# Kernel optimization log

Measured on AMD Instinct MI355X. Metric: run time of the kernel, lower is better.

## Reference

```python
import jax, jax.numpy as jnp
import numpy as np

B, S, E, H, D = 2, 2048, 512, 8, 64
NEG = -1e10


def setup_inputs() -> dict:
    key = jax.random.key(0)
    k1, k2, k3, k4, k5, k6 = jax.random.split(key, 6)
    inputs = jax.random.normal(k1, (B, S, E), dtype=jnp.float32)
    keys = jax.random.normal(k2, (B, S, H, D), dtype=jnp.float32)
    values = jax.random.normal(k3, (B, S, H, D), dtype=jnp.float32)
    # xavier-uniform style scale for square weights
    lim = float(np.sqrt(6.0 / (E + H * D)))
    query_weights = jax.random.uniform(k4, (E, H * D), minval=-lim, maxval=lim, dtype=jnp.float32)
    output_weights = jax.random.uniform(k5, (H * D, E), minval=-lim, maxval=lim, dtype=jnp.float32)
    mask = jax.random.randint(k6, (B, S, S), 0, 2).astype(jnp.bool_)
    return {"inputs": inputs, "keys": keys, "values": values,
            "query_weights": query_weights, "output_weights": output_weights,
            "mask": mask}


def reference(inputs, keys, values, query_weights, output_weights, mask):
    # project queries: (B,S,E) @ (E,H*D) -> (B,S,H,D)
    q = jnp.matmul(inputs, query_weights).reshape(B, S, H, D)
    # scores: (B,H,Sq,Sk)
    scores = jnp.einsum('bqhd,bkhd->bhqk', q, keys) / jnp.sqrt(jnp.float32(D))
    # masked_fill(mask, -1e10); mask broadcasts over heads
    scores = jnp.where(mask[:, None, :, :], jnp.float32(NEG), scores)
    probs = jax.nn.softmax(scores, axis=-1)
    # (B,H,Sq,Sk) x (B,Sk,H,D) -> (B,Sq,H,D)
    out = jnp.einsum('bhqk,bkhd->bqhd', probs, values)
    out = out.reshape(B, S, H * D)
    return jnp.matmul(out, output_weights)
```

## Files before the change

kernel.cpp:

```cpp
#include <hip/hip_runtime.h>
#include <hip/hip_bf16.h>

namespace {

constexpr int B = 2, S = 2048, E = 512, H = 8, D = 64, HD = 512;
constexpr float SL = 0.125f * 1.44269504f;
constexpr int PLD = 40;

typedef __attribute__((ext_vector_type(8))) short bf16x8;
typedef __attribute__((ext_vector_type(4))) unsigned short u16x4;
typedef __attribute__((ext_vector_type(4))) float f32x4;
typedef __attribute__((ext_vector_type(4))) float float4v;

__device__ __forceinline__ ushort f2b(float x) {
  __hip_bfloat16 h = __float2bfloat16(x);
  return *reinterpret_cast<const ushort*>(&h);
}

__global__ __launch_bounds__(256) void prep_fused_kernel(
    const float* __restrict__ K, const float* __restrict__ V,
    const float* __restrict__ Wq, const float* __restrict__ Wo,
    const int* __restrict__ maskp,
    ushort* __restrict__ Kbf, ushort* __restrict__ Vtbf,
    ushort* __restrict__ Wtq, ushort* __restrict__ Wto,
    uint4* __restrict__ keep4) {
  const int bid = blockIdx.x;
  const int t = threadIdx.x;
  if (bid < 512) {
    __shared__ __align__(16) ushort Vn[64][76];
    const int kt = bid & 31;
    const int bh = bid >> 5;
    const int b = bh >> 3, h = bh & 7;
    const int k0 = kt * 64;
#pragma unroll
    for (int i = 0; i < 4; ++i) {
      int c = i * 256 + t;
      int kk = c >> 4, d4 = (c & 15) * 4;
      size_t g = ((size_t)(b * 2048 + k0 + kk) * 8 + h) * 64 + d4;
      float4v kv = *(const float4v*)(K + g);
      float4v vv = *(const float4v*)(V + g);
      u16x4 kp = {f2b(kv.x), f2b(kv.y), f2b(kv.z), f2b(kv.w)};
      u16x4 vp = {f2b(vv.x), f2b(vv.y), f2b(vv.z), f2b(vv.w)};
      *(u16x4*)(Kbf + ((size_t)(bh * 2048 + k0 + kk)) * 64 + d4) = kp;
      *(u16x4*)&Vn[kk][d4] = vp;
    }
    __syncthreads();
#pragma unroll
    for (int i = 0; i < 2; ++i) {
      int c = i * 256 + t;
      int kc8 = (c & 7) * 8, d = c >> 3;
      union { ushort u[8]; bf16x8 v; } p;
#pragma unroll
      for (int j = 0; j < 8; ++j) p.u[j] = Vn[kc8 + j][d];
      *(bf16x8*)(Vtbf + ((size_t)(bh * 64 + d)) * 2048 + k0 + kc8) = p.v;
    }
  } else if (bid < 640) {
    __shared__ __align__(16) ushort T[64][68];
    const int idx = bid - 512;
    const float* Wsrc = (idx >> 6) ? Wo : Wq;
    ushort* Wdst = (idx >> 6) ? Wto : Wtq;
    const int x = idx & 63;
    const int k0 = (x & 7) * 64, n0 = (x >> 3) * 64;
#pragma unroll
    for (int i = 0; i < 4; ++i) {
      int c = i * 256 + t;
      int kk = c >> 4, n4 = (c & 15) * 4;
      float4v v = *(const float4v*)(Wsrc + (size_t)(k0 + kk) * 512 + n0 + n4);
      u16x4 p = {f2b(v.x), f2b(v.y), f2b(v.z), f2b(v.w)};
      *(u16x4*)&T[kk][n4] = p;
    }
    __syncthreads();
#pragma unroll
    for (int i = 0; i < 2; ++i) {
      int c = i * 256 + t;
      int n = c >> 3, k8 = (c & 7) * 8;
      union { ushort u[8]; bf16x8 v; } p;
#pragma unroll
      for (int j = 0; j < 8; ++j) p.u[j] = T[k8 + j][n];
      *(bf16x8*)(Wdst + (size_t)(n0 + n) * 512 + k0 + k8) = p.v;
    }
  } else {
    const int wid = (bid - 640) * 4 + (t >> 6);
    const int row = wid >> 3, c = wid & 7;
    const int lane = t & 63;
    const int4 v = *((const int4*)(maskp + (size_t)row * 2048 + c * 256) + lane);
    unsigned long long bx = __ballot(v.x == 0);
    unsigned long long by = __ballot(v.y == 0);
    unsigned long long bz = __ballot(v.z == 0);
    unsigned long long bw = __ballot(v.w == 0);
    if (lane == 0)
      keep4[(size_t)row * 16 + c * 2] = uint4{(uint)bx, (uint)by, (uint)bz, (uint)bw};
    if (lane == 32)
      keep4[(size_t)row * 16 + c * 2 + 1] =
          uint4{(uint)(bx >> 32), (uint)(by >> 32), (uint)(bz >> 32), (uint)(bw >> 32)};
  }
}

__global__ __launch_bounds__(256) void proj_out_kernel(
    const ushort* __restrict__ A, const ushort* __restrict__ Wt, float* __restrict__ C) {
  __shared__ __align__(16) ushort As[64][PLD];
  __shared__ __align__(16) ushort Ws[64][PLD];

  const int tid = threadIdx.x;
  const int lane = tid & 63;
  const int w = tid >> 6;
  const int col = lane & 15;
  const int quad = lane >> 4;
  const int m0 = blockIdx.y * 64;
  const int n0 = blockIdx.x * 64;
  const int wm = (w & 1) * 32;
  const int wn = (w >> 1) * 32;
  const int ar = tid >> 2;
  const int ak = (tid & 3) * 8;
  const int wn2 = tid >> 2;
  const int wkc = (tid & 3) * 8;

  f32x4 acc[2][2];
#pragma unroll
  for (int i = 0; i < 2; ++i)
#pragma unroll
    for (int j = 0; j < 2; ++j) acc[i][j] = f32x4{0.f, 0.f, 0.f, 0.f};

  const ushort* Ap = A + (size_t)(m0 + ar) * 512 + ak;
  const ushort* Wp = Wt + (size_t)(n0 + wn2) * 512 + wkc;
  bf16x8 apre = *(const bf16x8*)Ap;
  bf16x8 wp = *(const bf16x8*)Wp;

  for (int kt = 0; kt < 16; ++kt) {
    if (kt) __syncthreads();
    *(bf16x8*)&As[ar][ak] = apre;
    *(bf16x8*)&Ws[wn2][wkc] = wp;
    if (kt < 15) {
      const int k1 = (kt + 1) * 32;
      apre = *(const bf16x8*)(Ap + k1);
      wp = *(const bf16x8*)(Wp + k1);
    }
    __syncthreads();

    bf16x8 ah[2], wb[2];
#pragma unroll
    for (int i = 0; i < 2; ++i)
      ah[i] = *(const bf16x8*)&As[wm + i * 16 + col][quad * 8];
#pragma unroll
    for (int j = 0; j < 2; ++j)
      wb[j] = *(const bf16x8*)&Ws[wn + j * 16 + col][quad * 8];
#pragma unroll
    for (int i = 0; i < 2; ++i)
#pragma unroll
      for (int j = 0; j < 2; ++j)
        acc[i][j] = __builtin_amdgcn_mfma_f32_16x16x32_bf16(ah[i], wb[j], acc[i][j], 0, 0, 0);
  }

#pragma unroll
  for (int i = 0; i < 2; ++i)
#pragma unroll
    for (int j = 0; j < 2; ++j)
#pragma unroll
      for (int r = 0; r < 4; ++r)
        C[(size_t)(m0 + wm + i * 16 + (quad << 2) + r) * 512 + n0 + wn + j * 16 + col] =
            acc[i][j][r];
}

__global__ __launch_bounds__(256, 2) void flash_attn_kernel(
    const float* __restrict__ inp, const ushort* __restrict__ Wtq,
    const ushort* __restrict__ Kbf, const ushort* __restrict__ Vtbf,
    const uint4* __restrict__ keep4, ushort* __restrict__ Op) {
  __shared__ __align__(16) union SM {
    struct { ushort Ks[128][72]; ushort Vt[64][136]; ushort PQ[64][72]; } m;
    struct { float red[3][64][68]; float lred[3][64]; } r;
  } sm;

  const int bid = blockIdx.x;
  const int qt = bid & 31;
  const int bh = bid >> 5;
  const int b = bh >> 3, h = bh & 7;
  const int q0 = qt * 64;
  const int tid = threadIdx.x, lane = tid & 63, w = tid >> 6;
  const int col = lane & 15, quad = lane >> 4, quad4 = quad * 4;
  const int wm = (w & 1) * 32;
  const int wn = (w >> 1) * 32;

  {
    const int ar = tid >> 2;
    const int ak = (tid & 3) * 8;

    f32x4 qacc[2][2];
#pragma unroll
    for (int i = 0; i < 2; ++i)
#pragma unroll
      for (int j = 0; j < 2; ++j) qacc[i][j] = f32x4{0.f, 0.f, 0.f, 0.f};

    const float* Ap = inp + (size_t)(b * 2048 + q0 + ar) * 512 + ak;
    const ushort* Wp = Wtq + (size_t)(h * 64 + ar) * 512 + ak;
    float4v a0p = *(const float4v*)Ap;
    float4v a1p = *(const float4v*)(Ap + 4);
    bf16x8 wp = *(const bf16x8*)Wp;

    for (int kt = 0; kt < 16; ++kt) {
      if (kt) __syncthreads();
      {
        union { ushort u[8]; bf16x8 v; } ap;
        ap.u[0] = f2b(a0p.x); ap.u[1] = f2b(a0p.y); ap.u[2] = f2b(a0p.z); ap.u[3] = f2b(a0p.w);
        ap.u[4] = f2b(a1p.x); ap.u[5] = f2b(a1p.y); ap.u[6] = f2b(a1p.z); ap.u[7] = f2b(a1p.w);
        *(bf16x8*)&sm.m.PQ[ar][ak] = ap.v;
        *(bf16x8*)&sm.m.PQ[ar][40 + ak] = wp;
      }
      if (kt < 15) {
        const int k1 = (kt + 1) * 32;
        a0p = *(const float4v*)(Ap + k1);
        a1p = *(const float4v*)(Ap + k1 + 4);
        wp = *(const bf16x8*)(Wp + k1);
      }
      __syncthreads();

      bf16x8 ah[2], wb[2];
#pragma unroll
      for (int i = 0; i < 2; ++i)
        ah[i] = *(const bf16x8*)&sm.m.PQ[wm + i * 16 + col][quad * 8];
#pragma unroll
      for (int j = 0; j < 2; ++j)
        wb[j] = *(const bf16x8*)&sm.m.PQ[wn + j * 16 + col][40 + quad * 8];
#pragma unroll
      for (int i = 0; i < 2; ++i)
#pragma unroll
        for (int j = 0; j < 2; ++j)
          qacc[i][j] = __builtin_amdgcn_mfma_f32_16x16x32_bf16(ah[i], wb[j], qacc[i][j], 0, 0, 0);
    }

    __syncthreads();
#pragma unroll
    for (int i = 0; i < 2; ++i)
#pragma unroll
      for (int j = 0; j < 2; ++j)
#pragma unroll
        for (int r = 0; r < 4; ++r)
          sm.m.PQ[wm + i * 16 + quad4 + r][wn + j * 16 + col] = f2b(qacc[i][j][r]);
    __syncthreads();
  }

  bf16x8 qb[4][2];
#pragma unroll
  for (int j = 0; j < 4; ++j)
#pragma unroll
    for (int hf = 0; hf < 2; ++hf)
      qb[j][hf] = *(const bf16x8*)&sm.m.PQ[j * 16 + col][hf * 32 + quad * 8];

  f32x4 oacc[4][4];
#pragma unroll
  for (int j = 0; j < 4; ++j)
#pragma unroll
    for (int c = 0; c < 4; ++c) oacc[j][c] = f32x4{0.f, 0.f, 0.f, 0.f};
  f32x4 lacc[4];
#pragma unroll
  for (int j = 0; j < 4; ++j) lacc[j] = f32x4{0.f, 0.f, 0.f, 0.f};

  union { ushort u[8]; bf16x8 v; } onesu;
#pragma unroll
  for (int j = 0; j < 8; ++j) onesu.u[j] = 0x3F80;
  const bf16x8 onesB = onesu.v;

  const uint4* kr0 = keep4 + (size_t)(b * 2048 + q0 + col) * 16;
  const ushort* Kbase = Kbf + (size_t)bh * 2048 * 64;
  const ushort* Vbase = Vtbf + (size_t)bh * 64 * 2048;
  const int mshift = 8 * w + quad;

  bf16x8 kpre[4], vpre[4];
#pragma unroll
  for (int i = 0; i < 4; ++i) {
    int c = i * 256 + tid;
    kpre[i] = *(const bf16x8*)(Kbase + (size_t)c * 8);
    int d = c >> 4, k8 = (c & 15) * 8;
    vpre[i] = *(const bf16x8*)(Vbase + (size_t)d * 2048 + k8);
  }

  for (int kt = 0; kt < 16; ++kt) {
    if (kt) __syncthreads();
#pragma unroll
    for (int i = 0; i < 4; ++i) {
      int c = i * 256 + tid;
      *(bf16x8*)&sm.m.Ks[c >> 3][(c & 7) * 8] = kpre[i];
      int d = c >> 4, k8 = (c & 15) * 8;
      *(bf16x8*)&sm.m.Vt[d][k8] = vpre[i];
    }
    uint4 kwj[4];
#pragma unroll
    for (int j = 0; j < 4; ++j) kwj[j] = kr0[j * 256 + kt];
    if (kt < 15) {
      const int k1 = (kt + 1) * 128;
#pragma unroll
      for (int i = 0; i < 4; ++i) {
        int c = i * 256 + tid;
        kpre[i] = *(const bf16x8*)(Kbase + (size_t)k1 * 64 + c * 8);
        int d = c >> 4, k8 = (c & 15) * 8;
        vpre[i] = *(const bf16x8*)(Vbase + (size_t)d * 2048 + k1 + k8);
      }
    }
    __syncthreads();

    bf16x8 ka[2][2];
#pragma unroll
    for (int t = 0; t < 2; ++t)
#pragma unroll
      for (int hf = 0; hf < 2; ++hf)
        ka[t][hf] = *(const bf16x8*)&sm.m.Ks[w * 32 + t * 16 + col][hf * 32 + quad * 8];

    f32x4 sc[2][4];
#pragma unroll
    for (int t = 0; t < 2; ++t)
#pragma unroll
      for (int j = 0; j < 4; ++j) sc[t][j] = f32x4{0.f, 0.f, 0.f, 0.f};
#pragma unroll
    for (int t = 0; t < 2; ++t)
#pragma unroll
      for (int hf = 0; hf < 2; ++hf)
#pragma unroll
        for (int j = 0; j < 4; ++j)
          sc[t][j] = __builtin_amdgcn_mfma_f32_16x16x32_bf16(ka[t][hf], qb[j][hf], sc[t][j], 0, 0, 0);

    bf16x8 vb[4];
#pragma unroll
    for (int c = 0; c < 4; ++c)
      vb[c] = *(const bf16x8*)&sm.m.Vt[c * 16 + col][w * 32 + quad * 8];

#pragma unroll
    for (int j = 0; j < 4; ++j) {
      const uint mx_ = kwj[j].x >> mshift, my_ = kwj[j].y >> mshift,
                 mz_ = kwj[j].z >> mshift, mw_ = kwj[j].w >> mshift;
      uint Xa0, Xa1, Xb0, Xb1;
      {
        float p0 = (mx_ & 1u) ? exp2f(sc[0][j][0] * SL) : 0.f;
        float p1 = (my_ & 1u) ? exp2f(sc[0][j][1] * SL) : 0.f;
        float p2 = (mz_ & 1u) ? exp2f(sc[0][j][2] * SL) : 0.f;
        float p3 = (mw_ & 1u) ? exp2f(sc[0][j][3] * SL) : 0.f;
        __hip_bfloat162 lo = __float22bfloat162_rn(float2{p0, p1});
        __hip_bfloat162 hi = __float22bfloat162_rn(float2{p2, p3});
        Xa0 = *reinterpret_cast<uint*>(&lo);
        Xa1 = *reinterpret_cast<uint*>(&hi);
      }
      {
        float p0 = ((mx_ >> 4) & 1u) ? exp2f(sc[1][j][0] * SL) : 0.f;
        float p1 = ((my_ >> 4) & 1u) ? exp2f(sc[1][j][1] * SL) : 0.f;
        float p2 = ((mz_ >> 4) & 1u) ? exp2f(sc[1][j][2] * SL) : 0.f;
        float p3 = ((mw_ >> 4) & 1u) ? exp2f(sc[1][j][3] * SL) : 0.f;
        __hip_bfloat162 lo = __float22bfloat162_rn(float2{p0, p1});
        __hip_bfloat162 hi = __float22bfloat162_rn(float2{p2, p3});
        Xb0 = *reinterpret_cast<uint*>(&lo);
        Xb1 = *reinterpret_cast<uint*>(&hi);
      }
      auto a32 = __builtin_amdgcn_permlane32_swap(Xa0, Xb0, false, false);
      auto a16 = __builtin_amdgcn_permlane16_swap(a32[0], a32[1], false, false);
      auto b32 = __builtin_amdgcn_permlane32_swap(Xa1, Xb1, false, false);
      auto b16 = __builtin_amdgcn_permlane16_swap(b32[0], b32[1], false, false);
      union { uint u[4]; bf16x8 v; } pu;
      pu.u[0] = a16[0]; pu.u[1] = b16[0]; pu.u[2] = a16[1]; pu.u[3] = b16[1];
      const bf16x8 pa = pu.v;
      lacc[j] = __builtin_amdgcn_mfma_f32_16x16x32_bf16(pa, onesB, lacc[j], 0, 0, 0);
#pragma unroll
      for (int c = 0; c < 4; ++c)
        oacc[j][c] = __builtin_amdgcn_mfma_f32_16x16x32_bf16(pa, vb[c], oacc[j][c], 0, 0, 0);
    }
  }

  __syncthreads();
  if (w > 0) {
    const int wi = w - 1;
#pragma unroll
    for (int j = 0; j < 4; ++j)
#pragma unroll
      for (int c = 0; c < 4; ++c)
        *(f32x4*)&sm.r.red[wi][c * 16 + col][j * 16 + quad4] = oacc[j][c];
    if (col == 0)
#pragma unroll
      for (int j = 0; j < 4; ++j)
        *(f32x4*)&sm.r.lred[wi][j * 16 + quad4] = lacc[j];
  }
  __syncthreads();
  if (w == 0) {
#pragma unroll
    for (int j = 0; j < 4; ++j) {
#pragma unroll
      for (int c = 0; c < 4; ++c) {
        f32x4 s = oacc[j][c];
#pragma unroll
        for (int i = 0; i < 3; ++i)
          s += *(const f32x4*)&sm.r.red[i][c * 16 + col][j * 16 + quad4];
        oacc[j][c] = s;
      }
      f32x4 ls = lacc[j];
#pragma unroll
      for (int i = 0; i < 3; ++i)
        ls += *(const f32x4*)&sm.r.lred[i][j * 16 + quad4];
      lacc[j] = ls;
    }
#pragma unroll
    for (int j = 0; j < 4; ++j) {
#pragma unroll
      for (int c = 0; c < 4; ++c)
        *(f32x4*)&sm.r.red[0][c * 16 + col][j * 16 + quad4] = oacc[j][c];
      if (col == 0) *(f32x4*)&sm.r.lred[0][j * 16 + quad4] = lacc[j];
    }
  }
  __syncthreads();

  {
    const int q = tid >> 2, d0 = (tid & 3) * 16;
    const float inv = 1.f / sm.r.lred[0][q];
    union { ushort u[16]; bf16x8 v[2]; } ob;
#pragma unroll
    for (int dd = 0; dd < 16; ++dd)
      ob.u[dd] = f2b(sm.r.red[0][d0 + dd][q] * inv);
    ushort* dst = Op + (size_t)(b * S + q0 + q) * HD + h * D + d0;
    *(bf16x8*)dst = ob.v[0];
    *(bf16x8*)(dst + 8) = ob.v[1];
  }
}

}

extern "C" void kernel_launch(void* const* d_in, const int* in_sizes, int n_in,
                              void* d_out, int out_size, void* d_ws, size_t ws_size,
                              hipStream_t stream) {
  const float* inputs = (const float*)d_in[0];
  const float* keys   = (const float*)d_in[1];
  const float* values = (const float*)d_in[2];
  const float* wq     = (const float*)d_in[3];
  const float* wo     = (const float*)d_in[4];
  const int*   maskp  = (const int*)d_in[5];
  float* out = (float*)d_out;

  ushort* Kbf  = (ushort*)d_out;
  ushort* Vtbf = Kbf + (size_t)2097152;

  char* ws = (char*)d_ws;
  ushort* attnb = (ushort*)ws;
  uint4*  keep4 = (uint4*)(ws + (4 << 20));
  ushort* Wtq   = (ushort*)(ws + (5 << 20));
  ushort* Wto   = (ushort*)(ws + (5 << 20) + (512 << 10));

  prep_fused_kernel<<<dim3(8832), dim3(256), 0, stream>>>(keys, values, wq, wo, maskp,
                                                          Kbf, Vtbf, Wtq, Wto, keep4);
  flash_attn_kernel<<<dim3(512), dim3(256), 0, stream>>>(inputs, Wtq, Kbf, Vtbf, keep4, attnb);
  proj_out_kernel<<<dim3(8, 64), dim3(256), 0, stream>>>(attnb, Wto, out);
}
```

Measured before the change: 161.0 us.

## Halve attention query tile to 32 rows and double grid with block swizzle

The fused Q-projection and flash-attention kernel now processes 32 query rows per block instead of 64. The grid doubles to 1024 blocks and the launch-bounds occupancy target rises from 2 to 3, to fill the GPU better. Block indices are swizzled, the softmax scale is folded into Q when it is written to shared memory, the next tile's mask words are prefetched, and s_setprio is placed around the MFMA groups. The trade-off is that K/V tiles are loaded twice as often per query row, and half the threads sit idle while A is staged during the projection.

```diff
diff --git a/kernel.cpp b/kernel.cpp
--- a/kernel.cpp
+++ b/kernel.cpp
@@ -161,98 +161,92 @@
             acc[i][j][r];
 }
 
-__global__ __launch_bounds__(256, 2) void flash_attn_kernel(
+__global__ __launch_bounds__(256, 3) void flash_attn_kernel(
     const float* __restrict__ inp, const ushort* __restrict__ Wtq,
     const ushort* __restrict__ Kbf, const ushort* __restrict__ Vtbf,
     const uint4* __restrict__ keep4, ushort* __restrict__ Op) {
   __shared__ __align__(16) union SM {
-    struct { ushort Ks[128][72]; ushort Vt[64][136]; ushort PQ[64][72]; } m;
-    struct { float red[3][64][68]; float lred[3][64]; } r;
+    struct { ushort Ks[128][72]; ushort Vt[64][136]; } m;
+    ushort PQ[64][72];
+    struct { float red[3][64][40]; float lred[3][40]; } r;
   } sm;
 
-  const int bid = blockIdx.x;
-  const int qt = bid & 31;
-  const int bh = bid >> 5;
+  const int bid0 = blockIdx.x;
+  const int bid = (bid0 & 7) * 128 + (bid0 >> 3);
+  const int qt = bid & 63;
+  const int bh = bid >> 6;
   const int b = bh >> 3, h = bh & 7;
-  const int q0 = qt * 64;
+  const int q0 = qt * 32;
   const int tid = threadIdx.x, lane = tid & 63, w = tid >> 6;
   const int col = lane & 15, quad = lane >> 4, quad4 = quad * 4;
-  const int wm = (w & 1) * 32;
-  const int wn = (w >> 1) * 32;
 
   {
+    const int wmq = (w & 1) * 16;
+    const int wnq = (w >> 1) * 32;
     const int ar = tid >> 2;
     const int ak = (tid & 3) * 8;
-
-    f32x4 qacc[2][2];
-#pragma unroll
-    for (int i = 0; i < 2; ++i)
-#pragma unroll
-      for (int j = 0; j < 2; ++j) qacc[i][j] = f32x4{0.f, 0.f, 0.f, 0.f};
-
-    const float* Ap = inp + (size_t)(b * 2048 + q0 + ar) * 512 + ak;
+    const bool astage = tid < 128;
+
+    f32x4 qacc[2];
+    qacc[0] = f32x4{0.f, 0.f, 0.f, 0.f};
+    qacc[1] = f32x4{0.f, 0.f, 0.f, 0.f};
+
+    const float* Ap = inp + (size_t)(b * 2048 + q0 + (ar & 31)) * 512 + ak;
     const ushort* Wp = Wtq + (size_t)(h * 64 + ar) * 512 + ak;
-    float4v a0p = *(const float4v*)Ap;
-    float4v a1p = *(const float4v*)(Ap + 4);
+    float4v a0p{}, a1p{};
+    if (astage) { a0p = *(const float4v*)Ap; a1p = *(const float4v*)(Ap + 4); }
     bf16x8 wp = *(const bf16x8*)Wp;
 
     for (int kt = 0; kt < 16; ++kt) {
       if (kt) __syncthreads();
-      {
+      if (astage) {
         union { ushort u[8]; bf16x8 v; } ap;
         ap.u[0] = f2b(a0p.x); ap.u[1] = f2b(a0p.y); ap.u[2] = f2b(a0p.z); ap.u[3] = f2b(a0p.w);
         ap.u[4] = f2b(a1p.x); ap.u[5] = f2b(a1p.y); ap.u[6] = f2b(a1p.z); ap.u[7] = f2b(a1p.w);
-        *(bf16x8*)&sm.m.PQ[ar][ak] = ap.v;
-        *(bf16x8*)&sm.m.PQ[ar][40 + ak] = wp;
-      }
+        *(bf16x8*)&sm.PQ[ar][ak] = ap.v;
+      }
+      *(bf16x8*)&sm.PQ[ar][40 + ak] = wp;
+      __syncthreads();
       if (kt < 15) {
         const int k1 = (kt + 1) * 32;
-        a0p = *(const float4v*)(Ap + k1);
-        a1p = *(const float4v*)(Ap + k1 + 4);
+        if (astage) {
+          a0p = *(const float4v*)(Ap + k1);
+          a1p = *(const float4v*)(Ap + k1 + 4);
+        }
         wp = *(const bf16x8*)(Wp + k1);
       }
-      __syncthreads();
-
-      bf16x8 ah[2], wb[2];
-#pragma unroll
-      for (int i = 0; i < 2; ++i)
-        ah[i] = *(const bf16x8*)&sm.m.PQ[wm + i * 16 + col][quad * 8];
-#pragma unroll
-      for (int j = 0; j < 2; ++j)
-        wb[j] = *(const bf16x8*)&sm.m.PQ[wn + j * 16 + col][40 + quad * 8];
-#pragma unroll
-      for (int i = 0; i < 2; ++i)
-#pragma unroll
-        for (int j = 0; j < 2; ++j)
-          qacc[i][j] = __builtin_amdgcn_mfma_f32_16x16x32_bf16(ah[i], wb[j], qacc[i][j], 0, 0, 0);
-    }
-
-    __syncthreads();
-#pragma unroll
-    for (int i = 0; i < 2; ++i)
-#pragma unroll
-      for (int j = 0; j < 2; ++j)
-#pragma unroll
-        for (int r = 0; r < 4; ++r)
-          sm.m.PQ[wm + i * 16 + quad4 + r][wn + j * 16 + col] = f2b(qacc[i][j][r]);
-    __syncthreads();
-  }
-
-  bf16x8 qb[4][2];
-#pragma unroll
-  for (int j = 0; j < 4; ++j)
+      bf16x8 ah = *(const bf16x8*)&sm.PQ[wmq + col][quad * 8];
+      bf16x8 wb0 = *(const bf16x8*)&sm.PQ[wnq + col][40 + quad * 8];
+      bf16x8 wb1 = *(const bf16x8*)&sm.PQ[wnq + 16 + col][40 + quad * 8];
+      qacc[0] = __builtin_amdgcn_mfma_f32_16x16x32_bf16(ah, wb0, qacc[0], 0, 0, 0);
+      qacc[1] = __builtin_amdgcn_mfma_f32_16x16x32_bf16(ah, wb1, qacc[1], 0, 0, 0);
+    }
+
+    __syncthreads();
+#pragma unroll
+    for (int j = 0; j < 2; ++j)
+#pragma unroll
+      for (int r = 0; r < 4; ++r)
+        sm.PQ[wmq + quad4 + r][wnq + j * 16 + col] = f2b(qacc[j][r] * SL);
+    __syncthreads();
+  }
+
+  bf16x8 qb[2][2];
+#pragma unroll
+  for (int j = 0; j < 2; ++j)
 #pragma unroll
     for (int hf = 0; hf < 2; ++hf)
-      qb[j][hf] = *(const bf16x8*)&sm.m.PQ[j * 16 + col][hf * 32 + quad * 8];
-
-  f32x4 oacc[4][4];
-#pragma unroll
-  for (int j = 0; j < 4; ++j)
+      qb[j][hf] = *(const bf16x8*)&sm.PQ[j * 16 + col][hf * 32 + quad * 8];
+  __syncthreads();
+
+  f32x4 oacc[2][4];
+#pragma unroll
+  for (int j = 0; j < 2; ++j)
 #pragma unroll
     for (int c = 0; c < 4; ++c) oacc[j][c] = f32x4{0.f, 0.f, 0.f, 0.f};
-  f32x4 lacc[4];
-#pragma unroll
-  for (int j = 0; j < 4; ++j) lacc[j] = f32x4{0.f, 0.f, 0.f, 0.f};
+  f32x4 lacc[2];
+  lacc[0] = f32x4{0.f, 0.f, 0.f, 0.f};
+  lacc[1] = f32x4{0.f, 0.f, 0.f, 0.f};
 
   union { ushort u[8]; bf16x8 v; } onesu;
 #pragma unroll
@@ -265,6 +259,7 @@
   const int mshift = 8 * w + quad;
 
   bf16x8 kpre[4], vpre[4];
+  uint4 kwj[2];
 #pragma unroll
   for (int i = 0; i < 4; ++i) {
     int c = i * 256 + tid;
@@ -272,6 +267,8 @@
     int d = c >> 4, k8 = (c & 15) * 8;
     vpre[i] = *(const bf16x8*)(Vbase + (size_t)d * 2048 + k8);
   }
+  kwj[0] = kr0[0];
+  kwj[1] = kr0[256];
 
   for (int kt = 0; kt < 16; ++kt) {
     if (kt) __syncthreads();
@@ -282,9 +279,9 @@
       int d = c >> 4, k8 = (c & 15) * 8;
       *(bf16x8*)&sm.m.Vt[d][k8] = vpre[i];
     }
-    uint4 kwj[4];
-#pragma unroll
-    for (int j = 0; j < 4; ++j) kwj[j] = kr0[j * 256 + kt];
+    __syncthreads();
+
+    uint4 kwn0 = kwj[0], kwn1 = kwj[1];
     if (kt < 15) {
       const int k1 = (kt + 1) * 128;
 #pragma unroll
@@ -294,8 +291,9 @@
         int d = c >> 4, k8 = (c & 15) * 8;
         vpre[i] = *(const bf16x8*)(Vbase + (size_t)d * 2048 + k1 + k8);
       }
-    }
-    __syncthreads();
+      kwn0 = kr0[kt + 1];
+      kwn1 = kr0[256 + kt + 1];
+    }
 
     bf16x8 ka[2][2];
 #pragma unroll
@@ -304,18 +302,20 @@
       for (int hf = 0; hf < 2; ++hf)
         ka[t][hf] = *(const bf16x8*)&sm.m.Ks[w * 32 + t * 16 + col][hf * 32 + quad * 8];
 
-    f32x4 sc[2][4];
+    f32x4 sc[2][2];
 #pragma unroll
     for (int t = 0; t < 2; ++t)
 #pragma unroll
-      for (int j = 0; j < 4; ++j) sc[t][j] = f32x4{0.f, 0.f, 0.f, 0.f};
+      for (int j = 0; j < 2; ++j) sc[t][j] = f32x4{0.f, 0.f, 0.f, 0.f};
+    __builtin_amdgcn_s_setprio(1);
 #pragma unroll
     for (int t = 0; t < 2; ++t)
 #pragma unroll
       for (int hf = 0; hf < 2; ++hf)
 #pragma unroll
-        for (int j = 0; j < 4; ++j)
+        for (int j = 0; j < 2; ++j)
           sc[t][j] = __builtin_amdgcn_mfma_f32_16x16x32_bf16(ka[t][hf], qb[j][hf], sc[t][j], 0, 0, 0);
+    __builtin_amdgcn_s_setprio(0);
 
     bf16x8 vb[4];
 #pragma unroll
@@ -323,25 +323,26 @@
       vb[c] = *(const bf16x8*)&sm.m.Vt[c * 16 + col][w * 32 + quad * 8];
 
 #pragma unroll
-    for (int j = 0; j < 4; ++j) {
-      const uint mx_ = kwj[j].x >> mshift, my_ = kwj[j].y >> mshift,
-                 mz_ = kwj[j].z >> mshift, mw_ = kwj[j].w >> mshift;
+    for (int j = 0; j < 2; ++j) {
+      const uint4 kwv = j ? kwn1 * 0 + kwj[1] : kwj[0];
+      const uint mx_ = kwv.x >> mshift, my_ = kwv.y >> mshift,
+                 mz_ = kwv.z >> mshift, mw_ = kwv.w >> mshift;
       uint Xa0, Xa1, Xb0, Xb1;
       {
-        float p0 = (mx_ & 1u) ? exp2f(sc[0][j][0] * SL) : 0.f;
-        float p1 = (my_ & 1u) ? exp2f(sc[0][j][1] * SL) : 0.f;
-        float p2 = (mz_ & 1u) ? exp2f(sc[0][j][2] * SL) : 0.f;
-        float p3 = (mw_ & 1u) ? exp2f(sc[0][j][3] * SL) : 0.f;
+        float p0 = (mx_ & 1u) ? exp2f(sc[0][j][0]) : 0.f;
+        float p1 = (my_ & 1u) ? exp2f(sc[0][j][1]) : 0.f;
+        float p2 = (mz_ & 1u) ? exp2f(sc[0][j][2]) : 0.f;
+        float p3 = (mw_ & 1u) ? exp2f(sc[0][j][3]) : 0.f;
         __hip_bfloat162 lo = __float22bfloat162_rn(float2{p0, p1});
         __hip_bfloat162 hi = __float22bfloat162_rn(float2{p2, p3});
         Xa0 = *reinterpret_cast<uint*>(&lo);
         Xa1 = *reinterpret_cast<uint*>(&hi);
       }
       {
-        float p0 = ((mx_ >> 4) & 1u) ? exp2f(sc[1][j][0] * SL) : 0.f;
-        float p1 = ((my_ >> 4) & 1u) ? exp2f(sc[1][j][1] * SL) : 0.f;
-        float p2 = ((mz_ >> 4) & 1u) ? exp2f(sc[1][j][2] * SL) : 0.f;
-        float p3 = ((mw_ >> 4) & 1u) ? exp2f(sc[1][j][3] * SL) : 0.f;
+        float p0 = ((mx_ >> 4) & 1u) ? exp2f(sc[1][j][0]) : 0.f;
+        float p1 = ((my_ >> 4) & 1u) ? exp2f(sc[1][j][1]) : 0.f;
+        float p2 = ((mz_ >> 4) & 1u) ? exp2f(sc[1][j][2]) : 0.f;
+        float p3 = ((mw_ >> 4) & 1u) ? exp2f(sc[1][j][3]) : 0.f;
         __hip_bfloat162 lo = __float22bfloat162_rn(float2{p0, p1});
         __hip_bfloat162 hi = __float22bfloat162_rn(float2{p2, p3});
         Xb0 = *reinterpret_cast<uint*>(&lo);
@@ -354,30 +355,32 @@
       union { uint u[4]; bf16x8 v; } pu;
       pu.u[0] = a16[0]; pu.u[1] = b16[0]; pu.u[2] = a16[1]; pu.u[3] = b16[1];
       const bf16x8 pa = pu.v;
+      __builtin_amdgcn_s_setprio(1);
       lacc[j] = __builtin_amdgcn_mfma_f32_16x16x32_bf16(pa, onesB, lacc[j], 0, 0, 0);
 #pragma unroll
       for (int c = 0; c < 4; ++c)
         oacc[j][c] = __builtin_amdgcn_mfma_f32_16x16x32_bf16(pa, vb[c], oacc[j][c], 0, 0, 0);
-    }
+      __builtin_amdgcn_s_setprio(0);
+    }
+    kwj[0] = kwn0;
+    kwj[1] = kwn1;
   }
 
   __syncthreads();
   if (w > 0) {
     const int wi = w - 1;
 #pragma unroll
-    for (int j = 0; j < 4; ++j)
+    for (int j = 0; j < 2; ++j) {
 #pragma unroll
       for (int c = 0; c < 4; ++c)
         *(f32x4*)&sm.r.red[wi][c * 16 + col][j * 16 + quad4] = oacc[j][c];
-    if (col == 0)
-#pragma unroll
-      for (int j = 0; j < 4; ++j)
-        *(f32x4*)&sm.r.lred[wi][j * 16 + quad4] = lacc[j];
+      if (col == 0) *(f32x4*)&sm.r.lred[wi][j * 16 + quad4] = lacc[j];
+    }
   }
   __syncthreads();
   if (w == 0) {
 #pragma unroll
-    for (int j = 0; j < 4; ++j) {
+    for (int j = 0; j < 2; ++j) {
 #pragma unroll
       for (int c = 0; c < 4; ++c) {
         f32x4 s = oacc[j][c];
@@ -393,7 +396,7 @@
       lacc[j] = ls;
     }
 #pragma unroll
-    for (int j = 0; j < 4; ++j) {
+    for (int j = 0; j < 2; ++j) {
 #pragma unroll
       for (int c = 0; c < 4; ++c)
         *(f32x4*)&sm.r.red[0][c * 16 + col][j * 16 + quad4] = oacc[j][c];
@@ -403,15 +406,14 @@
   __syncthreads();
 
   {
-    const int q = tid >> 2, d0 = (tid & 3) * 16;
+    const int q = tid >> 3, d0 = (tid & 7) * 8;
     const float inv = 1.f / sm.r.lred[0][q];
-    union { ushort u[16]; bf16x8 v[2]; } ob;
-#pragma unroll
-    for (int dd = 0; dd < 16; ++dd)
+    union { ushort u[8]; bf16x8 v; } ob;
+#pragma unroll
+    for (int dd = 0; dd < 8; ++dd)
       ob.u[dd] = f2b(sm.r.red[0][d0 + dd][q] * inv);
     ushort* dst = Op + (size_t)(b * S + q0 + q) * HD + h * D + d0;
-    *(bf16x8*)dst = ob.v[0];
-    *(bf16x8*)(dst + 8) = ob.v[1];
+    *(bf16x8*)dst = ob.v;
   }
 }
 
@@ -439,6 +441,6 @@
 
   prep_fused_kernel<<<dim3(8832), dim3(256), 0, stream>>>(keys, values, wq, wo, maskp,
                                                           Kbf, Vtbf, Wtq, Wto, keep4);
-  flash_attn_kernel<<<dim3(512), dim3(256), 0, stream>>>(inputs, Wtq, Kbf, Vtbf, keep4, attnb);
+  flash_attn_kernel<<<dim3(1024), dim3(256), 0, stream>>>(inputs, Wtq, Kbf, Vtbf, keep4, attnb);
   proj_out_kernel<<<dim3(8, 64), dim3(256), 0, stream>>>(attnb, Wto, out);
 }
```

Result: slower. 169.7 us (+5.4%).

## Load K/V fragments directly from global into registers, drop LDS staging

Applied to the files above, without the earlier changes.

The attention loop no longer stages K and V tiles through shared memory with block-wide barriers. Each wave instead reads its MFMA fragments straight from global memory, with register double-buffering of K and mask words across iterations. The softmax scale is folded into Q when it is written to LDS, which removes a multiply per score. Block indices are also remapped so that consecutive blocks spread across batch/head. This removes LDS traffic and barriers at the cost of redundant global/L2 reads of V across waves and higher register pressure.

```diff
diff --git a/kernel.cpp b/kernel.cpp
--- a/kernel.cpp
+++ b/kernel.cpp
@@ -166,11 +166,12 @@
     const ushort* __restrict__ Kbf, const ushort* __restrict__ Vtbf,
     const uint4* __restrict__ keep4, ushort* __restrict__ Op) {
   __shared__ __align__(16) union SM {
-    struct { ushort Ks[128][72]; ushort Vt[64][136]; ushort PQ[64][72]; } m;
+    ushort PQ[64][72];
     struct { float red[3][64][68]; float lred[3][64]; } r;
   } sm;
 
-  const int bid = blockIdx.x;
+  const int bid0 = blockIdx.x;
+  const int bid = (bid0 & 7) * 64 + (bid0 >> 3);
   const int qt = bid & 31;
   const int bh = bid >> 5;
   const int b = bh >> 3, h = bh & 7;
@@ -202,8 +203,8 @@
         union { ushort u[8]; bf16x8 v; } ap;
         ap.u[0] = f2b(a0p.x); ap.u[1] = f2b(a0p.y); ap.u[2] = f2b(a0p.z); ap.u[3] = f2b(a0p.w);
         ap.u[4] = f2b(a1p.x); ap.u[5] = f2b(a1p.y); ap.u[6] = f2b(a1p.z); ap.u[7] = f2b(a1p.w);
-        *(bf16x8*)&sm.m.PQ[ar][ak] = ap.v;
-        *(bf16x8*)&sm.m.PQ[ar][40 + ak] = wp;
+        *(bf16x8*)&sm.PQ[ar][ak] = ap.v;
+        *(bf16x8*)&sm.PQ[ar][40 + ak] = wp;
       }
       if (kt < 15) {
         const int k1 = (kt + 1) * 32;
@@ -216,10 +217,10 @@
       bf16x8 ah[2], wb[2];
 #pragma unroll
       for (int i = 0; i < 2; ++i)
-        ah[i] = *(const bf16x8*)&sm.m.PQ[wm + i * 16 + col][quad * 8];
+        ah[i] = *(const bf16x8*)&sm.PQ[wm + i * 16 + col][quad * 8];
 #pragma unroll
       for (int j = 0; j < 2; ++j)
-        wb[j] = *(const bf16x8*)&sm.m.PQ[wn + j * 16 + col][40 + quad * 8];
+        wb[j] = *(const bf16x8*)&sm.PQ[wn + j * 16 + col][40 + quad * 8];
 #pragma unroll
       for (int i = 0; i < 2; ++i)
 #pragma unroll
@@ -234,7 +235,7 @@
       for (int j = 0; j < 2; ++j)
 #pragma unroll
         for (int r = 0; r < 4; ++r)
-          sm.m.PQ[wm + i * 16 + quad4 + r][wn + j * 16 + col] = f2b(qacc[i][j][r]);
+          sm.PQ[wm + i * 16 + quad4 + r][wn + j * 16 + col] = f2b(qacc[i][j][r] * SL);
     __syncthreads();
   }
 
@@ -243,7 +244,7 @@
   for (int j = 0; j < 4; ++j)
 #pragma unroll
     for (int hf = 0; hf < 2; ++hf)
-      qb[j][hf] = *(const bf16x8*)&sm.m.PQ[j * 16 + col][hf * 32 + quad * 8];
+      qb[j][hf] = *(const bf16x8*)&sm.PQ[j * 16 + col][hf * 32 + quad * 8];
 
   f32x4 oacc[4][4];
 #pragma unroll
@@ -260,88 +261,54 @@
   const bf16x8 onesB = onesu.v;
 
   const uint4* kr0 = keep4 + (size_t)(b * 2048 + q0 + col) * 16;
-  const ushort* Kbase = Kbf + (size_t)bh * 2048 * 64;
-  const ushort* Vbase = Vtbf + (size_t)bh * 64 * 2048;
+  const ushort* Kp = Kbf + (size_t)bh * 131072 + (size_t)(w * 32 + col) * 64 + quad * 8;
+  const ushort* Vp = Vtbf + (size_t)bh * 131072 + (size_t)col * 2048 + w * 32 + quad * 8;
   const int mshift = 8 * w + quad;
 
-  bf16x8 kpre[4], vpre[4];
-#pragma unroll
-  for (int i = 0; i < 4; ++i) {
-    int c = i * 256 + tid;
-    kpre[i] = *(const bf16x8*)(Kbase + (size_t)c * 8);
-    int d = c >> 4, k8 = (c & 15) * 8;
-    vpre[i] = *(const bf16x8*)(Vbase + (size_t)d * 2048 + k8);
-  }
-
-  for (int kt = 0; kt < 16; ++kt) {
-    if (kt) __syncthreads();
-#pragma unroll
-    for (int i = 0; i < 4; ++i) {
-      int c = i * 256 + tid;
-      *(bf16x8*)&sm.m.Ks[c >> 3][(c & 7) * 8] = kpre[i];
-      int d = c >> 4, k8 = (c & 15) * 8;
-      *(bf16x8*)&sm.m.Vt[d][k8] = vpre[i];
-    }
-    uint4 kwj[4];
-#pragma unroll
-    for (int j = 0; j < 4; ++j) kwj[j] = kr0[j * 256 + kt];
-    if (kt < 15) {
-      const int k1 = (kt + 1) * 128;
-#pragma unroll
-      for (int i = 0; i < 4; ++i) {
-        int c = i * 256 + tid;
-        kpre[i] = *(const bf16x8*)(Kbase + (size_t)k1 * 64 + c * 8);
-        int d = c >> 4, k8 = (c & 15) * 8;
-        vpre[i] = *(const bf16x8*)(Vbase + (size_t)d * 2048 + k1 + k8);
-      }
-    }
-    __syncthreads();
-
-    bf16x8 ka[2][2];
+  auto LOADK = [&](bf16x8 (&d)[2][2], const int kt) {
 #pragma unroll
     for (int t = 0; t < 2; ++t)
 #pragma unroll
       for (int hf = 0; hf < 2; ++hf)
-        ka[t][hf] = *(const bf16x8*)&sm.m.Ks[w * 32 + t * 16 + col][hf * 32 + quad * 8];
-
-    f32x4 sc[2][4];
-#pragma unroll
-    for (int t = 0; t < 2; ++t)
-#pragma unroll
-      for (int j = 0; j < 4; ++j) sc[t][j] = f32x4{0.f, 0.f, 0.f, 0.f};
-#pragma unroll
-    for (int t = 0; t < 2; ++t)
-#pragma unroll
-      for (int hf = 0; hf < 2; ++hf)
-#pragma unroll
-        for (int j = 0; j < 4; ++j)
-          sc[t][j] = __builtin_amdgcn_mfma_f32_16x16x32_bf16(ka[t][hf], qb[j][hf], sc[t][j], 0, 0, 0);
-
-    bf16x8 vb[4];
-#pragma unroll
-    for (int c = 0; c < 4; ++c)
-      vb[c] = *(const bf16x8*)&sm.m.Vt[c * 16 + col][w * 32 + quad * 8];
-
+        d[t][hf] = *(const bf16x8*)(Kp + kt * 8192 + t * 1024 + hf * 32);
+  };
+  auto LOADM = [&](uint4 (&d)[4], const int kt) {
+#pragma unroll
+    for (int j = 0; j < 4; ++j) d[j] = kr0[j * 256 + kt];
+  };
+  auto COMPUTE = [&](const bf16x8 (&ka)[2][2], const uint4 (&kwj)[4], const int kt) {
+    bf16x8 vv[4];
 #pragma unroll
     for (int j = 0; j < 4; ++j) {
+      f32x4 sc0 = f32x4{0.f, 0.f, 0.f, 0.f};
+      f32x4 sc1 = f32x4{0.f, 0.f, 0.f, 0.f};
+      sc0 = __builtin_amdgcn_mfma_f32_16x16x32_bf16(ka[0][0], qb[j][0], sc0, 0, 0, 0);
+      sc0 = __builtin_amdgcn_mfma_f32_16x16x32_bf16(ka[0][1], qb[j][1], sc0, 0, 0, 0);
+      sc1 = __builtin_amdgcn_mfma_f32_16x16x32_bf16(ka[1][0], qb[j][0], sc1, 0, 0, 0);
+      sc1 = __builtin_amdgcn_mfma_f32_16x16x32_bf16(ka[1][1], qb[j][1], sc1, 0, 0, 0);
+      if (j == 0) {
+#pragma unroll
+        for (int c = 0; c < 4; ++c)
+          vv[c] = *(const bf16x8*)(Vp + kt * 128 + c * 32768);
+      }
       const uint mx_ = kwj[j].x >> mshift, my_ = kwj[j].y >> mshift,
                  mz_ = kwj[j].z >> mshift, mw_ = kwj[j].w >> mshift;
       uint Xa0, Xa1, Xb0, Xb1;
       {
-        float p0 = (mx_ & 1u) ? exp2f(sc[0][j][0] * SL) : 0.f;
-        float p1 = (my_ & 1u) ? exp2f(sc[0][j][1] * SL) : 0.f;
-        float p2 = (mz_ & 1u) ? exp2f(sc[0][j][2] * SL) : 0.f;
-        float p3 = (mw_ & 1u) ? exp2f(sc[0][j][3] * SL) : 0.f;
+        float p0 = (mx_ & 1u) ? exp2f(sc0[0]) : 0.f;
+        float p1 = (my_ & 1u) ? exp2f(sc0[1]) : 0.f;
+        float p2 = (mz_ & 1u) ? exp2f(sc0[2]) : 0.f;
+        float p3 = (mw_ & 1u) ? exp2f(sc0[3]) : 0.f;
         __hip_bfloat162 lo = __float22bfloat162_rn(float2{p0, p1});
         __hip_bfloat162 hi = __float22bfloat162_rn(float2{p2, p3});
         Xa0 = *reinterpret_cast<uint*>(&lo);
         Xa1 = *reinterpret_cast<uint*>(&hi);
       }
       {
-        float p0 = ((mx_ >> 4) & 1u) ? exp2f(sc[1][j][0] * SL) : 0.f;
-        float p1 = ((my_ >> 4) & 1u) ? exp2f(sc[1][j][1] * SL) : 0.f;
-        float p2 = ((mz_ >> 4) & 1u) ? exp2f(sc[1][j][2] * SL) : 0.f;
-        float p3 = ((mw_ >> 4) & 1u) ? exp2f(sc[1][j][3] * SL) : 0.f;
+        float p0 = ((mx_ >> 4) & 1u) ? exp2f(sc1[0]) : 0.f;
+        float p1 = ((my_ >> 4) & 1u) ? exp2f(sc1[1]) : 0.f;
+        float p2 = ((mz_ >> 4) & 1u) ? exp2f(sc1[2]) : 0.f;
+        float p3 = ((mw_ >> 4) & 1u) ? exp2f(sc1[3]) : 0.f;
         __hip_bfloat162 lo = __float22bfloat162_rn(float2{p0, p1});
         __hip_bfloat162 hi = __float22bfloat162_rn(float2{p2, p3});
         Xb0 = *reinterpret_cast<uint*>(&lo);
@@ -357,8 +324,21 @@
       lacc[j] = __builtin_amdgcn_mfma_f32_16x16x32_bf16(pa, onesB, lacc[j], 0, 0, 0);
 #pragma unroll
       for (int c = 0; c < 4; ++c)
-        oacc[j][c] = __builtin_amdgcn_mfma_f32_16x16x32_bf16(pa, vb[c], oacc[j][c], 0, 0, 0);
-    }
+        oacc[j][c] = __builtin_amdgcn_mfma_f32_16x16x32_bf16(pa, vv[c], oacc[j][c], 0, 0, 0);
+    }
+  };
+
+  bf16x8 kA[2][2], kB[2][2];
+  uint4 kwA[4], kwB[4];
+  LOADK(kA, 0);
+#pragma unroll 1
+  for (int kt = 0; kt < 16; kt += 2) {
+    LOADM(kwA, kt);
+    LOADK(kB, kt + 1);
+    COMPUTE(kA, kwA, kt);
+    LOADM(kwB, kt + 1);
+    if (kt < 14) LOADK(kA, kt + 2);
+    COMPUTE(kB, kwB, kt + 1);
   }
 
   __syncthreads();
```

Result: slower. 168.4 us (+4.6%).

## Move Q projection into prep kernel and prescale Q by softmax scale

Applied to the files above, without the earlier changes.

The Q projection (inputs @ Wq) moves out of the flash attention kernel into new blocks of the prep kernel. Those blocks write Q in bf16, already multiplied by the softmax scale, in a per-head layout that the attention kernel reads straight from global memory. This removes duplicated projection work and the PQ shared buffer from attention, and drops one multiply per exp. It also adds s_setprio around the MFMA sections. The cost is an extra global round-trip for Q and a prep kernel whose Wq is transposed through shared memory with scattered ushort stores.

```diff
diff --git a/kernel.cpp b/kernel.cpp
--- a/kernel.cpp
+++ b/kernel.cpp
@@ -18,11 +18,12 @@
 }
 
 __global__ __launch_bounds__(256) void prep_fused_kernel(
+    const float* __restrict__ inp,
     const float* __restrict__ K, const float* __restrict__ V,
     const float* __restrict__ Wq, const float* __restrict__ Wo,
     const int* __restrict__ maskp,
     ushort* __restrict__ Kbf, ushort* __restrict__ Vtbf,
-    ushort* __restrict__ Wtq, ushort* __restrict__ Wto,
+    ushort* __restrict__ Wto, ushort* __restrict__ Qbf,
     uint4* __restrict__ keep4) {
   const int bid = blockIdx.x;
   const int t = threadIdx.x;
@@ -54,18 +55,15 @@
       for (int j = 0; j < 8; ++j) p.u[j] = Vn[kc8 + j][d];
       *(bf16x8*)(Vtbf + ((size_t)(bh * 64 + d)) * 2048 + k0 + kc8) = p.v;
     }
-  } else if (bid < 640) {
+  } else if (bid < 576) {
     __shared__ __align__(16) ushort T[64][68];
-    const int idx = bid - 512;
-    const float* Wsrc = (idx >> 6) ? Wo : Wq;
-    ushort* Wdst = (idx >> 6) ? Wto : Wtq;
-    const int x = idx & 63;
+    const int x = bid - 512;
     const int k0 = (x & 7) * 64, n0 = (x >> 3) * 64;
 #pragma unroll
     for (int i = 0; i < 4; ++i) {
       int c = i * 256 + t;
       int kk = c >> 4, n4 = (c & 15) * 4;
-      float4v v = *(const float4v*)(Wsrc + (size_t)(k0 + kk) * 512 + n0 + n4);
+      float4v v = *(const float4v*)(Wo + (size_t)(k0 + kk) * 512 + n0 + n4);
       u16x4 p = {f2b(v.x), f2b(v.y), f2b(v.z), f2b(v.w)};
       *(u16x4*)&T[kk][n4] = p;
     }
@@ -77,10 +75,10 @@
       union { ushort u[8]; bf16x8 v; } p;
 #pragma unroll
       for (int j = 0; j < 8; ++j) p.u[j] = T[k8 + j][n];
-      *(bf16x8*)(Wdst + (size_t)(n0 + n) * 512 + k0 + k8) = p.v;
-    }
-  } else {
-    const int wid = (bid - 640) * 4 + (t >> 6);
+      *(bf16x8*)(Wto + (size_t)(n0 + n) * 512 + k0 + k8) = p.v;
+    }
+  } else if (bid < 8768) {
+    const int wid = (bid - 576) * 4 + (t >> 6);
     const int row = wid >> 3, c = wid & 7;
     const int lane = t & 63;
     const int4 v = *((const int4*)(maskp + (size_t)row * 2048 + c * 256) + lane);
@@ -93,6 +91,77 @@
     if (lane == 32)
       keep4[(size_t)row * 16 + c * 2 + 1] =
           uint4{(uint)(bx >> 32), (uint)(by >> 32), (uint)(bz >> 32), (uint)(bw >> 32)};
+  } else {
+    __shared__ __align__(16) ushort As[64][PLD];
+    __shared__ __align__(16) ushort Ws[64][PLD];
+    const int idx = bid - 8768;
+    const int m0 = (idx >> 3) * 64;
+    const int n0 = (idx & 7) * 64;
+    const int lane = t & 63, w = t >> 6;
+    const int col = lane & 15, quad = lane >> 4, quad4 = quad * 4;
+    const int wm = (w & 1) * 32, wn = (w >> 1) * 32;
+    const int ar = t >> 2, ak = (t & 3) * 8;
+    const int wk = t & 31, wn8 = (t >> 5) * 8;
+
+    f32x4 acc[2][2];
+#pragma unroll
+    for (int i = 0; i < 2; ++i)
+#pragma unroll
+      for (int j = 0; j < 2; ++j) acc[i][j] = f32x4{0.f, 0.f, 0.f, 0.f};
+
+    const float* Ap = inp + (size_t)(m0 + ar) * 512 + ak;
+    const float* Wp = Wq + (size_t)wk * 512 + n0 + wn8;
+    float4v a0 = *(const float4v*)Ap;
+    float4v a1 = *(const float4v*)(Ap + 4);
+    float4v w0 = *(const float4v*)Wp;
+    float4v w1 = *(const float4v*)(Wp + 4);
+
+    for (int kt = 0; kt < 16; ++kt) {
+      if (kt) __syncthreads();
+      {
+        union { ushort u[8]; bf16x8 v; } ap;
+        ap.u[0] = f2b(a0.x); ap.u[1] = f2b(a0.y); ap.u[2] = f2b(a0.z); ap.u[3] = f2b(a0.w);
+        ap.u[4] = f2b(a1.x); ap.u[5] = f2b(a1.y); ap.u[6] = f2b(a1.z); ap.u[7] = f2b(a1.w);
+        *(bf16x8*)&As[ar][ak] = ap.v;
+        ushort wu[8] = {f2b(w0.x), f2b(w0.y), f2b(w0.z), f2b(w0.w),
+                        f2b(w1.x), f2b(w1.y), f2b(w1.z), f2b(w1.w)};
+#pragma unroll
+        for (int i = 0; i < 8; ++i) Ws[wn8 + i][wk] = wu[i];
+      }
+      if (kt < 15) {
+        const int k1 = (kt + 1) * 32;
+        a0 = *(const float4v*)(Ap + k1);
+        a1 = *(const float4v*)(Ap + k1 + 4);
+        w0 = *(const float4v*)(Wp + (size_t)k1 * 512);
+        w1 = *(const float4v*)(Wp + (size_t)k1 * 512 + 4);
+      }
+      __syncthreads();
+
+      bf16x8 ah[2], wb[2];
+#pragma unroll
+      for (int i = 0; i < 2; ++i)
+        ah[i] = *(const bf16x8*)&As[wm + i * 16 + col][quad * 8];
+#pragma unroll
+      for (int j = 0; j < 2; ++j)
+        wb[j] = *(const bf16x8*)&Ws[wn + j * 16 + col][quad * 8];
+#pragma unroll
+      for (int i = 0; i < 2; ++i)
+#pragma unroll
+        for (int j = 0; j < 2; ++j)
+          acc[i][j] = __builtin_amdgcn_mfma_f32_16x16x32_bf16(ah[i], wb[j], acc[i][j], 0, 0, 0);
+    }
+
+#pragma unroll
+    for (int i = 0; i < 2; ++i)
+#pragma unroll
+      for (int j = 0; j < 2; ++j)
+#pragma unroll
+        for (int r = 0; r < 4; ++r) {
+          int m = m0 + wm + i * 16 + quad4 + r;
+          int n = n0 + wn + j * 16 + col;
+          int b = m >> 11, q = m & 2047, h = n >> 6, dd = n & 63;
+          Qbf[((size_t)(b * 8 + h) * 2048 + q) * 64 + dd] = f2b(acc[i][j][r] * SL);
+        }
   }
 }
 
@@ -162,11 +231,11 @@
 }
 
 __global__ __launch_bounds__(256, 2) void flash_attn_kernel(
-    const float* __restrict__ inp, const ushort* __restrict__ Wtq,
+    const ushort* __restrict__ Qbf,
     const ushort* __restrict__ Kbf, const ushort* __restrict__ Vtbf,
     const uint4* __restrict__ keep4, ushort* __restrict__ Op) {
   __shared__ __align__(16) union SM {
-    struct { ushort Ks[128][72]; ushort Vt[64][136]; ushort PQ[64][72]; } m;
+    struct { ushort Ks[128][72]; ushort Vt[64][136]; } m;
     struct { float red[3][64][68]; float lred[3][64]; } r;
   } sm;
 
@@ -177,73 +246,14 @@
   const int q0 = qt * 64;
   const int tid = threadIdx.x, lane = tid & 63, w = tid >> 6;
   const int col = lane & 15, quad = lane >> 4, quad4 = quad * 4;
-  const int wm = (w & 1) * 32;
-  const int wn = (w >> 1) * 32;
-
-  {
-    const int ar = tid >> 2;
-    const int ak = (tid & 3) * 8;
-
-    f32x4 qacc[2][2];
-#pragma unroll
-    for (int i = 0; i < 2; ++i)
-#pragma unroll
-      for (int j = 0; j < 2; ++j) qacc[i][j] = f32x4{0.f, 0.f, 0.f, 0.f};
-
-    const float* Ap = inp + (size_t)(b * 2048 + q0 + ar) * 512 + ak;
-    const ushort* Wp = Wtq + (size_t)(h * 64 + ar) * 512 + ak;
-    float4v a0p = *(const float4v*)Ap;
-    float4v a1p = *(const float4v*)(Ap + 4);
-    bf16x8 wp = *(const bf16x8*)Wp;
-
-    for (int kt = 0; kt < 16; ++kt) {
-      if (kt) __syncthreads();
-      {
-        union { ushort u[8]; bf16x8 v; } ap;
-        ap.u[0] = f2b(a0p.x); ap.u[1] = f2b(a0p.y); ap.u[2] = f2b(a0p.z); ap.u[3] = f2b(a0p.w);
-        ap.u[4] = f2b(a1p.x); ap.u[5] = f2b(a1p.y); ap.u[6] = f2b(a1p.z); ap.u[7] = f2b(a1p.w);
-        *(bf16x8*)&sm.m.PQ[ar][ak] = ap.v;
-        *(bf16x8*)&sm.m.PQ[ar][40 + ak] = wp;
-      }
-      if (kt < 15) {
-        const int k1 = (kt + 1) * 32;
-        a0p = *(const float4v*)(Ap + k1);
-        a1p = *(const float4v*)(Ap + k1 + 4);
-        wp = *(const bf16x8*)(Wp + k1);
-      }
-      __syncthreads();
-
-      bf16x8 ah[2], wb[2];
-#pragma unroll
-      for (int i = 0; i < 2; ++i)
-        ah[i] = *(const bf16x8*)&sm.m.PQ[wm + i * 16 + col][quad * 8];
-#pragma unroll
-      for (int j = 0; j < 2; ++j)
-        wb[j] = *(const bf16x8*)&sm.m.PQ[wn + j * 16 + col][40 + quad * 8];
-#pragma unroll
-      for (int i = 0; i < 2; ++i)
-#pragma unroll
-        for (int j = 0; j < 2; ++j)
-          qacc[i][j] = __builtin_amdgcn_mfma_f32_16x16x32_bf16(ah[i], wb[j], qacc[i][j], 0, 0, 0);
-    }
-
-    __syncthreads();
-#pragma unroll
-    for (int i = 0; i < 2; ++i)
-#pragma unroll
-      for (int j = 0; j < 2; ++j)
-#pragma unroll
-        for (int r = 0; r < 4; ++r)
-          sm.m.PQ[wm + i * 16 + quad4 + r][wn + j * 16 + col] = f2b(qacc[i][j][r]);
-    __syncthreads();
-  }
-
+
+  const ushort* Qt = Qbf + (size_t)(bh * 2048 + q0) * 64;
   bf16x8 qb[4][2];
 #pragma unroll
   for (int j = 0; j < 4; ++j)
 #pragma unroll
     for (int hf = 0; hf < 2; ++hf)
-      qb[j][hf] = *(const bf16x8*)&sm.m.PQ[j * 16 + col][hf * 32 + quad * 8];
+      qb[j][hf] = *(const bf16x8*)(Qt + (j * 16 + col) * 64 + hf * 32 + quad * 8);
 
   f32x4 oacc[4][4];
 #pragma unroll
@@ -260,8 +270,8 @@
   const bf16x8 onesB = onesu.v;
 
   const uint4* kr0 = keep4 + (size_t)(b * 2048 + q0 + col) * 16;
-  const ushort* Kbase = Kbf + (size_t)bh * 2048 * 64;
-  const ushort* Vbase = Vtbf + (size_t)bh * 64 * 2048;
+  const ushort* Kbase = Kbf + (size_t)bh * 131072;
+  const ushort* Vbase = Vtbf + (size_t)bh * 131072;
   const int mshift = 8 * w + quad;
 
   bf16x8 kpre[4], vpre[4];
@@ -309,6 +319,7 @@
     for (int t = 0; t < 2; ++t)
 #pragma unroll
       for (int j = 0; j < 4; ++j) sc[t][j] = f32x4{0.f, 0.f, 0.f, 0.f};
+    __builtin_amdgcn_s_setprio(1);
 #pragma unroll
     for (int t = 0; t < 2; ++t)
 #pragma unroll
@@ -316,6 +327,7 @@
 #pragma unroll
         for (int j = 0; j < 4; ++j)
           sc[t][j] = __builtin_amdgcn_mfma_f32_16x16x32_bf16(ka[t][hf], qb[j][hf], sc[t][j], 0, 0, 0);
+    __builtin_amdgcn_s_setprio(0);
 
     bf16x8 vb[4];
 #pragma unroll
@@ -328,20 +340,20 @@
                  mz_ = kwj[j].z >> mshift, mw_ = kwj[j].w >> mshift;
       uint Xa0, Xa1, Xb0, Xb1;
       {
-        float p0 = (mx_ & 1u) ? exp2f(sc[0][j][0] * SL) : 0.f;
-        float p1 = (my_ & 1u) ? exp2f(sc[0][j][1] * SL) : 0.f;
-        float p2 = (mz_ & 1u) ? exp2f(sc[0][j][2] * SL) : 0.f;
-        float p3 = (mw_ & 1u) ? exp2f(sc[0][j][3] * SL) : 0.f;
+        float p0 = (mx_ & 1u) ? exp2f(sc[0][j][0]) : 0.f;
+        float p1 = (my_ & 1u) ? exp2f(sc[0][j][1]) : 0.f;
+        float p2 = (mz_ & 1u) ? exp2f(sc[0][j][2]) : 0.f;
+        float p3 = (mw_ & 1u) ? exp2f(sc[0][j][3]) : 0.f;
         __hip_bfloat162 lo = __float22bfloat162_rn(float2{p0, p1});
         __hip_bfloat162 hi = __float22bfloat162_rn(float2{p2, p3});
         Xa0 = *reinterpret_cast<uint*>(&lo);
         Xa1 = *reinterpret_cast<uint*>(&hi);
       }
       {
-        float p0 = ((mx_ >> 4) & 1u) ? exp2f(sc[1][j][0] * SL) : 0.f;
-        float p1 = ((my_ >> 4) & 1u) ? exp2f(sc[1][j][1] * SL) : 0.f;
-        float p2 = ((mz_ >> 4) & 1u) ? exp2f(sc[1][j][2] * SL) : 0.f;
-        float p3 = ((mw_ >> 4) & 1u) ? exp2f(sc[1][j][3] * SL) : 0.f;
+        float p0 = ((mx_ >> 4) & 1u) ? exp2f(sc[1][j][0]) : 0.f;
+        float p1 = ((my_ >> 4) & 1u) ? exp2f(sc[1][j][1]) : 0.f;
+        float p2 = ((mz_ >> 4) & 1u) ? exp2f(sc[1][j][2]) : 0.f;
+        float p3 = ((mw_ >> 4) & 1u) ? exp2f(sc[1][j][3]) : 0.f;
         __hip_bfloat162 lo = __float22bfloat162_rn(float2{p0, p1});
         __hip_bfloat162 hi = __float22bfloat162_rn(float2{p2, p3});
         Xb0 = *reinterpret_cast<uint*>(&lo);
@@ -354,10 +366,12 @@
       union { uint u[4]; bf16x8 v; } pu;
       pu.u[0] = a16[0]; pu.u[1] = b16[0]; pu.u[2] = a16[1]; pu.u[3] = b16[1];
       const bf16x8 pa = pu.v;
+      __builtin_amdgcn_s_setprio(1);
       lacc[j] = __builtin_amdgcn_mfma_f32_16x16x32_bf16(pa, onesB, lacc[j], 0, 0, 0);
 #pragma unroll
       for (int c = 0; c < 4; ++c)
         oacc[j][c] = __builtin_amdgcn_mfma_f32_16x16x32_bf16(pa, vb[c], oacc[j][c], 0, 0, 0);
+      __builtin_amdgcn_s_setprio(0);
     }
   }
 
@@ -432,13 +446,13 @@
   ushort* Vtbf = Kbf + (size_t)2097152;
 
   char* ws = (char*)d_ws;
-  ushort* attnb = (ushort*)ws;
-  uint4*  keep4 = (uint4*)(ws + (4 << 20));
-  ushort* Wtq   = (ushort*)(ws + (5 << 20));
-  ushort* Wto   = (ushort*)(ws + (5 << 20) + (512 << 10));
-
-  prep_fused_kernel<<<dim3(8832), dim3(256), 0, stream>>>(keys, values, wq, wo, maskp,
-                                                          Kbf, Vtbf, Wtq, Wto, keep4);
-  flash_attn_kernel<<<dim3(512), dim3(256), 0, stream>>>(inputs, Wtq, Kbf, Vtbf, keep4, attnb);
+  ushort* Qbf   = (ushort*)ws;
+  ushort* attnb = (ushort*)(ws + (4 << 20));
+  uint4*  keep4 = (uint4*)(ws + (8 << 20));
+  ushort* Wto   = (ushort*)(ws + (9 << 20));
+
+  prep_fused_kernel<<<dim3(9280), dim3(256), 0, stream>>>(
+      inputs, keys, values, wq, wo, maskp, Kbf, Vtbf, Wto, Qbf, keep4);
+  flash_attn_kernel<<<dim3(512), dim3(256), 0, stream>>>(Qbf, Kbf, Vtbf, keep4, attnb);
   proj_out_kernel<<<dim3(8, 64), dim3(256), 0, stream>>>(attnb, Wto, out);
 }
```

New measurement: 175.9 us. 9.3% more time.
